# Performance work log

Hardware: AMD Instinct MI355X
Metric: run time of the kernel (lower is better)

## Reference

```python
import jax, jax.numpy as jnp
import numpy as np

NUM_HEADS = 8
FREQ_RATIO = 0.5

def setup_inputs() -> dict:
    key = jax.random.key(0)
    ks = jax.random.split(key, 4)
    B, T, J, C = 16, 256, 17, 512
    x = jax.random.normal(ks[0], (B, T, J, C), jnp.float32)
    w_qkv = jax.random.normal(ks[1], (3 * C, C), jnp.float32) * 0.02
    w_proj = jax.random.normal(ks[2], (C, C), jnp.float32) * 0.02
    b_proj = jnp.zeros((C,), jnp.float32)
    freq_gate = jnp.ones((1,), jnp.float32)
    return {"x": x, "w_qkv": w_qkv, "w_proj": w_proj, "b_proj": b_proj, "freq_gate": freq_gate}

def reference(x, w_qkv, w_proj, b_proj, freq_gate):
    B, T, J, C = x.shape
    H = NUM_HEADS
    hd = C // H
    scale = hd ** (-0.5)
    # qkv projection (no bias): [B,T,J,3,H,hd] -> [3,B,H,T,J,hd]
    qkv = (x @ w_qkv.T).reshape(B, T, J, 3, H, hd)
    qkv = jnp.transpose(qkv, (3, 0, 4, 1, 2, 5))
    q, k, v = qkv[0], qkv[1], qkv[2]
    # temporal layout: [B,H,J,T,hd]
    qt = jnp.swapaxes(q, 2, 3)
    kt = jnp.swapaxes(k, 2, 3)
    vt = jnp.swapaxes(v, 2, 3)
    # ---- time-domain temporal attention ----
    attn = jax.nn.softmax(jnp.einsum('bhjtd,bhjsd->bhjts', qt, kt) * scale, axis=-1)
    x_time = jnp.einsum('bhjts,bhjsd->bhjtd', attn, vt)
    x_time = jnp.transpose(x_time, (0, 3, 2, 1, 4)).reshape(B, T, J, C)
    # ---- frequency-domain temporal attention ----
    qf = jnp.fft.rfft(qt, axis=3)
    kf = jnp.fft.rfft(kt, axis=3)
    vf = jnp.fft.rfft(vt, axis=3)
    f_full = T // 2 + 1
    keep = max(1, int(f_full * FREQ_RATIO))  # low-frequency crop
    qf, kf, vf = qf[:, :, :, :keep], kf[:, :, :, :keep], vf[:, :, :, :keep]
    af = jnp.einsum('bhjfd,bhjgd->bhjfg', qf, jnp.conj(kf)) * scale  # complex [B,H,J,keep,keep]
    af = jax.nn.softmax(af.real, axis=-1) + 1j * jax.nn.softmax(af.imag, axis=-1)
    xf = jnp.einsum('bhjfg,bhjgd->bhjfd', af, vf)
    xf = jnp.pad(xf, ((0, 0), (0, 0), (0, 0), (0, f_full - keep), (0, 0)))  # zero-pad high freqs
    x_freq = jnp.fft.irfft(xf, n=T, axis=3)
    x_freq = jnp.transpose(x_freq, (0, 3, 2, 1, 4)).reshape(B, T, J, C)
    # ---- gated combine + output projection ----
    gate = jax.nn.sigmoid(freq_gate)[0]
    out = gate * x_freq + (1.0 - gate) * x_time
    return out @ w_proj.T + b_proj
```

## Files before the change

### kernel.cpp

```cpp
#include <hip/hip_runtime.h>
#include <hip/hip_fp16.h>
#include <math.h>

#define NB 16
#define TT 256
#define JJ 17
#define CC 512
#define HH 8
#define HD 64
#define MROWS (NB*TT*JJ)
#define QTILE 16384
#define NTILES (NB*HH*JJ)
#define NQKV 35651584

#define W0 0.0245436926061702596f

typedef __attribute__((ext_vector_type(8))) short i16x8;
typedef __attribute__((ext_vector_type(8))) _Float16 f16x8;
typedef __attribute__((ext_vector_type(4))) float f32x4;

__device__ __forceinline__ unsigned short f2h(float f) {
    return (unsigned short)__half_as_ushort(__float2half(f));
}
__device__ __forceinline__ float h2f(unsigned short u) {
    return __half2float(__ushort_as_half(u));
}

#define GLD16(gp, lp) __builtin_amdgcn_global_load_lds( \
    (__attribute__((address_space(1))) void*)(gp), \
    (__attribute__((address_space(3))) void*)(lp), 16, 0, 0)

__global__ __launch_bounds__(256) void conv16_k(
    const float* __restrict__ s, unsigned short* __restrict__ d, int n8)
{
    for (int i = blockIdx.x*256 + threadIdx.x; i < n8; i += gridDim.x*256) {
        float4 a = ((const float4*)s)[i*2];
        float4 b = ((const float4*)s)[i*2+1];
        i16x8 h;
        h[0] = (short)f2h(a.x); h[1] = (short)f2h(a.y);
        h[2] = (short)f2h(a.z); h[3] = (short)f2h(a.w);
        h[4] = (short)f2h(b.x); h[5] = (short)f2h(b.y);
        h[6] = (short)f2h(b.z); h[7] = (short)f2h(b.w);
        ((i16x8*)d)[i] = h;
    }
}

__global__ __launch_bounds__(256) void prep_k(
    const float* __restrict__ wq, const float* __restrict__ wp,
    unsigned short* __restrict__ wqh, unsigned short* __restrict__ wph,
    unsigned short* __restrict__ Whi, unsigned short* __restrict__ Wlo,
    unsigned short* __restrict__ WIhi)
{
    const int b = blockIdx.x;
    const int tid = threadIdx.x;
    if (b < 512) {
        const float* s = (b < 384) ? wq : wp;
        unsigned short* d = (b < 384) ? wqh : wph;
        int i = (b < 384 ? b : b - 384)*256 + tid;
        float4 a = ((const float4*)s)[i*2];
        float4 bb = ((const float4*)s)[i*2+1];
        i16x8 h;
        h[0] = (short)f2h(a.x); h[1] = (short)f2h(a.y);
        h[2] = (short)f2h(a.z); h[3] = (short)f2h(a.w);
        h[4] = (short)f2h(bb.x); h[5] = (short)f2h(bb.y);
        h[6] = (short)f2h(bb.z); h[7] = (short)f2h(bb.w);
        ((i16x8*)d)[i] = h;
    } else if (b < 640) {
        const int r = b - 512;
        const int t = tid;
        int idx = ((r & 63) * t) & 255;
        float sv, cv;
        sincosf(W0 * (float)idx, &sv, &cv);
        float val = (r < 64) ? cv : -sv;
        unsigned short h = f2h(val);
        Whi[r*256 + t] = h;
        Wlo[r*256 + t] = f2h(val - h2f(h));
    } else {
        int idx = (b - 640)*256 + tid;
        int t = idx >> 7;
        int f = idx & 127;
        int fr = f & 63;
        int ii = (t * fr) & 255;
        float sv, cv;
        sincosf(W0 * (float)ii, &sv, &cv);
        float cf = (fr == 0 && f < 64) ? 0.5f : 1.f;
        float val = ((f < 64) ? cv : -sv) * cf * (2.f / 256.f);
        WIhi[t*128 + f] = f2h(val);
    }
}

__global__ __launch_bounds__(256) void gemm_qkv_k(
    const unsigned short* __restrict__ A, const unsigned short* __restrict__ B,
    unsigned short* __restrict__ qp, unsigned short* __restrict__ kp,
    unsigned short* __restrict__ vp)
{
    __shared__ unsigned short Sh[128*128];
    unsigned short* Ah = Sh;
    unsigned short* Bh = Sh + 128*64;
    const int tid = threadIdx.x;
    const int lane = tid & 63;
    const int lo = lane & 15, hi = lane >> 4;
    const int wv = tid >> 6;
    const int wr = wv >> 1, wc = wv & 1;
    const int bid = blockIdx.x;
    const int wrk = (bid & 7) * 816 + (bid >> 3);
    const int col0 = (wrk % 12) * 128;
    const int row0 = (wrk / 12) * 128;

    f32x4 acc[4][4];
    #pragma unroll
    for (int rb = 0; rb < 4; ++rb)
        #pragma unroll
        for (int cb = 0; cb < 4; ++cb) acc[rb][cb] = (f32x4){0.f,0.f,0.f,0.f};

    for (int k0 = 0; k0 < 512; k0 += 64) {
        #pragma unroll
        for (int c = 0; c < 4; ++c) {
            int e = c*2048 + tid*8;
            int r = e >> 6, cc = e & 63;
            int ccs = cc ^ ((r & 7) << 3);
            size_t offA = (size_t)(row0 + r)*512 + k0 + ccs;
            size_t offB = (size_t)(col0 + r)*512 + k0 + ccs;
            GLD16(A + offA, (char*)Ah + c*4096 + tid*16);
            GLD16(B + offB, (char*)Bh + c*4096 + tid*16);
        }
        __syncthreads();
        #pragma unroll
        for (int ks = 0; ks < 2; ++ks) {
            f16x8 af[4], bf[4];
            #pragma unroll
            for (int rb = 0; rb < 4; ++rb) {
                int row = wr*64 + rb*16 + lo;
                int col = (ks*32 + hi*8) ^ ((row & 7) << 3);
                af[rb] = *(const f16x8*)&Ah[row*64 + col];
            }
            #pragma unroll
            for (int cb = 0; cb < 4; ++cb) {
                int row = wc*64 + cb*16 + lo;
                int col = (ks*32 + hi*8) ^ ((row & 7) << 3);
                bf[cb] = *(const f16x8*)&Bh[row*64 + col];
            }
            #pragma unroll
            for (int rb = 0; rb < 4; ++rb)
                #pragma unroll
                for (int cb = 0; cb < 4; ++cb)
                    acc[rb][cb] = __builtin_amdgcn_mfma_f32_16x16x32_f16(
                        af[rb], bf[cb], acc[rb][cb], 0, 0, 0);
        }
        __syncthreads();
    }

    #pragma unroll
    for (int cb = 0; cb < 4; ++cb) {
        int n0 = col0 + wc*64 + cb*16;
        float scl = ((n0 >> 9) == 0) ? 0.125f : 1.f;
        #pragma unroll
        for (int rb = 0; rb < 4; ++rb)
            #pragma unroll
            for (int r = 0; r < 4; ++r) {
                int row = wr*64 + rb*16 + hi*4 + r;
                int col = wc*64 + cb*16 + lo;
                Sh[row*128 + (col ^ ((row & 7) << 3))] = f2h(acc[rb][cb][r]*scl);
            }
    }
    __syncthreads();

    {
        const int grp = lane >> 3;
        const int d0 = (lane & 7) * 8;
        #pragma unroll
        for (int it = 0; it < 8; ++it) {
            int p = it*32 + wv*8 + grp;
            int row = p >> 1;
            int half = p & 1;
            int m = row0 + row;
            int bb = m / (TT*JJ);
            int rem = m - bb*(TT*JJ);
            int t = rem / JJ;
            int j = rem - t*JJ;
            int n0 = col0 + half*64;
            int g = n0 >> 9;
            unsigned short* dst0 = (g == 0) ? qp : (g == 1) ? kp : vp;
            int h = (n0 >> 6) & 7;
            unsigned short* dst = dst0 +
                ((((size_t)bb*HH + h)*JJ + j)*TT + t)*HD + d0;
            i16x8 vls = *(const i16x8*)&Sh[row*128 + ((half*64 + d0) ^ ((row & 7) << 3))];
            *(i16x8*)dst = vls;
        }
    }
}

__global__ __launch_bounds__(256) void gemm_proj_k(
    const unsigned short* __restrict__ A, const unsigned short* __restrict__ B,
    const float* __restrict__ bias, float* __restrict__ out)
{
    __shared__ unsigned short Ah[128*64];
    __shared__ unsigned short Bh[128*64];
    const int tid = threadIdx.x;
    const int lane = tid & 63;
    const int lo = lane & 15, hi = lane >> 4;
    const int wv = tid >> 6;
    const int wr = wv >> 1, wc = wv & 1;
    const int bid = blockIdx.x;
    const int wrk = (bid & 7) * 272 + (bid >> 3);
    const int col0 = (wrk % 4) * 128;
    const int row0 = (wrk / 4) * 128;

    f32x4 acc[4][4];
    #pragma unroll
    for (int rb = 0; rb < 4; ++rb)
        #pragma unroll
        for (int cb = 0; cb < 4; ++cb) acc[rb][cb] = (f32x4){0.f,0.f,0.f,0.f};

    for (int k0 = 0; k0 < 512; k0 += 64) {
        #pragma unroll
        for (int c = 0; c < 4; ++c) {
            int e = c*2048 + tid*8;
            int r = e >> 6, cc = e & 63;
            int ccs = cc ^ ((r & 7) << 3);
            size_t offA = (size_t)(row0 + r)*512 + k0 + ccs;
            size_t offB = (size_t)(col0 + r)*512 + k0 + ccs;
            GLD16(A + offA, (char*)Ah + c*4096 + tid*16);
            GLD16(B + offB, (char*)Bh + c*4096 + tid*16);
        }
        __syncthreads();
        #pragma unroll
        for (int ks = 0; ks < 2; ++ks) {
            f16x8 af[4], bf[4];
            #pragma unroll
            for (int rb = 0; rb < 4; ++rb) {
                int row = wr*64 + rb*16 + lo;
                int col = (ks*32 + hi*8) ^ ((row & 7) << 3);
                af[rb] = *(const f16x8*)&Ah[row*64 + col];
            }
            #pragma unroll
            for (int cb = 0; cb < 4; ++cb) {
                int row = wc*64 + cb*16 + lo;
                int col = (ks*32 + hi*8) ^ ((row & 7) << 3);
                bf[cb] = *(const f16x8*)&Bh[row*64 + col];
            }
            #pragma unroll
            for (int rb = 0; rb < 4; ++rb)
                #pragma unroll
                for (int cb = 0; cb < 4; ++cb)
                    acc[rb][cb] = __builtin_amdgcn_mfma_f32_16x16x32_f16(
                        af[rb], bf[cb], acc[rb][cb], 0, 0, 0);
        }
        __syncthreads();
    }

    #pragma unroll
    for (int cb = 0; cb < 4; ++cb) {
        int n = col0 + wc*64 + cb*16 + lo;
        float bv = bias[n];
        #pragma unroll
        for (int rb = 0; rb < 4; ++rb)
            #pragma unroll
            for (int r = 0; r < 4; ++r) {
                int m = row0 + wr*64 + rb*16 + hi*4 + r;
                out[(size_t)m*512 + n] = acc[rb][cb][r] + bv;
            }
    }
}

#define PPW 40

__global__ __launch_bounds__(256, 3) void attn_time_k(
    const unsigned short* __restrict__ q, const unsigned short* __restrict__ k,
    const unsigned short* __restrict__ v, const float* __restrict__ fg,
    unsigned short* __restrict__ y)
{
    __shared__ unsigned short VT[64 * 256];
    __shared__ unsigned short PL[4 * 64 * PPW];

    const int bid = blockIdx.x;
    const int b = bid / (HH*JJ);
    const int h = (bid / JJ) % HH;
    const int j = bid % JJ;
    const size_t base = (size_t)bid * QTILE;

    const int tid = threadIdx.x;
    const int w = tid >> 6;
    const int lane = tid & 63;
    const int lo = lane & 15;
    const int hi = lane >> 4;

    {
        const unsigned short* vptr = v + base + (size_t)tid * HD;
        #pragma unroll
        for (int d0 = 0; d0 < 64; d0 += 8) {
            i16x8 vv = *(const i16x8*)(vptr + d0);
            #pragma unroll
            for (int e = 0; e < 8; ++e) {
                int row = d0 + e;
                VT[row*256 + (tid ^ ((row & 7) << 3))] = (unsigned short)vv[e];
            }
        }
    }
    __syncthreads();

    f16x8 qf[4][2];
    #pragma unroll
    for (int rb = 0; rb < 4; ++rb)
        #pragma unroll
        for (int dc = 0; dc < 2; ++dc)
            qf[rb][dc] = *(const f16x8*)(q + base + (size_t)(w*64 + rb*16 + lo)*HD + dc*32 + hi*8);

    f32x4 o[4][4];
    #pragma unroll
    for (int rb = 0; rb < 4; ++rb)
        #pragma unroll
        for (int cd = 0; cd < 4; ++cd) o[rb][cd] = (f32x4){0.f,0.f,0.f,0.f};
    float rs[4][4];
    #pragma unroll
    for (int rb = 0; rb < 4; ++rb)
        #pragma unroll
        for (int r = 0; r < 4; ++r) rs[rb][r] = 0.f;

    unsigned short* Pw = PL + w * 64 * PPW;

    for (int st = 0; st < 8; ++st) {
        const int s0 = st * 32;
        f16x8 kf[2][2];
        #pragma unroll
        for (int cb = 0; cb < 2; ++cb)
            #pragma unroll
            for (int dc = 0; dc < 2; ++dc)
                kf[cb][dc] = *(const f16x8*)(k + base + (size_t)(s0 + cb*16 + lo)*HD + dc*32 + hi*8);

        #pragma unroll
        for (int rb = 0; rb < 4; ++rb) {
            #pragma unroll
            for (int cb = 0; cb < 2; ++cb) {
                f32x4 acc = (f32x4){0.f,0.f,0.f,0.f};
                acc = __builtin_amdgcn_mfma_f32_16x16x32_f16(qf[rb][0], kf[cb][0], acc, 0, 0, 0);
                acc = __builtin_amdgcn_mfma_f32_16x16x32_f16(qf[rb][1], kf[cb][1], acc, 0, 0, 0);
                #pragma unroll
                for (int r = 0; r < 4; ++r) {
                    float p = __expf(acc[r]);
                    rs[rb][r] += p;
                    Pw[(rb*16 + hi*4 + r)*PPW + cb*16 + lo] = f2h(p);
                }
            }
        }

        f16x8 pa[4];
        #pragma unroll
        for (int rb = 0; rb < 4; ++rb)
            pa[rb] = *(const f16x8*)&Pw[(rb*16 + lo)*PPW + hi*8];
        f16x8 bv[4];
        #pragma unroll
        for (int cd = 0; cd < 4; ++cd) {
            int row = cd*16 + lo;
            bv[cd] = *(const f16x8*)&VT[row*256 + ((s0 + hi*8) ^ ((row & 7) << 3))];
        }
        #pragma unroll
        for (int rb = 0; rb < 4; ++rb)
            #pragma unroll
            for (int cd = 0; cd < 4; ++cd)
                o[rb][cd] = __builtin_amdgcn_mfma_f32_16x16x32_f16(pa[rb], bv[cd], o[rb][cd], 0, 0, 0);
    }

    #pragma unroll
    for (int off = 1; off < 16; off <<= 1)
        #pragma unroll
        for (int rb = 0; rb < 4; ++rb)
            #pragma unroll
            for (int r = 0; r < 4; ++r)
                rs[rb][r] += __shfl_xor(rs[rb][r], off, 64);

    const float gate = 1.f / (1.f + __expf(-fg[0]));
    const float wt = 1.f - gate;
    #pragma unroll
    for (int rb = 0; rb < 4; ++rb) {
        #pragma unroll
        for (int r = 0; r < 4; ++r) {
            const int t = w*64 + rb*16 + hi*4 + r;
            const float sc = wt / rs[rb][r];
            unsigned short* yp = y + (((size_t)b*TT + t)*JJ + j)*CC + h*HD;
            #pragma unroll
            for (int cd = 0; cd < 4; ++cd)
                yp[cd*16 + lo] = f2h(o[rb][cd][r] * sc);
        }
    }
}

#define XP 280

__global__ __launch_bounds__(256) void dft_k(
    unsigned short* __restrict__ planes, const unsigned short* __restrict__ Whi,
    const unsigned short* __restrict__ Wlo)
{
    __shared__ unsigned short Xh[64*XP];
    unsigned short* src = planes + (size_t)blockIdx.y*NQKV + (size_t)blockIdx.x*QTILE;
    const int tid = threadIdx.x;
    const int w = tid >> 6;
    const int lane = tid & 63;
    const int qd = (tid >> 4) & 3;
    const int rr = tid & 15;
    const int lo = lane & 15, hi = lane >> 4;

    #pragma unroll
    for (int p = 0; p < 16; ++p) {
        const int t = p*16 + 4*w + qd;
        ushort4 x4 = *(const ushort4*)&src[t*64 + 4*rr];
        unsigned int a0 = x4.x, a1 = x4.y, a2 = x4.z, a3 = x4.w;
        unsigned int t01 = (unsigned)__shfl_xor((int)((qd&1) ? a0 : a1), 16, 64);
        unsigned int t23 = (unsigned)__shfl_xor((int)((qd&1) ? a2 : a3), 16, 64);
        if (qd&1) { a0 = t01; a2 = t23; } else { a1 = t01; a3 = t23; }
        unsigned int u01 = (unsigned)__shfl_xor((int)((qd&2) ? a0 : a2), 32, 64);
        unsigned int u23 = (unsigned)__shfl_xor((int)((qd&2) ? a1 : a3), 32, 64);
        if (qd&2) { a0 = u01; a1 = u23; } else { a2 = u01; a3 = u23; }
        const int dd = 4*rr + qd;
        const int tb = p*16 + 4*w;
        ushort4 hv;
        hv.x = (unsigned short)a0; hv.y = (unsigned short)a1;
        hv.z = (unsigned short)a2; hv.w = (unsigned short)a3;
        *(ushort4*)&Xh[dd*XP + tb] = hv;
    }
    __syncthreads();

    f32x4 acc[2][4];
    #pragma unroll
    for (int rb = 0; rb < 2; ++rb)
        #pragma unroll
        for (int cd = 0; cd < 4; ++cd) acc[rb][cd] = (f32x4){0.f,0.f,0.f,0.f};

    for (int ks = 0; ks < 8; ++ks) {
        const int k0 = ks*32;
        f16x8 ah[2], al[2];
        #pragma unroll
        for (int rb = 0; rb < 2; ++rb) {
            int r = w*32 + rb*16 + lo;
            ah[rb] = *(const f16x8*)&Whi[r*256 + k0 + hi*8];
            al[rb] = *(const f16x8*)&Wlo[r*256 + k0 + hi*8];
        }
        f16x8 bh[4];
        #pragma unroll
        for (int cd = 0; cd < 4; ++cd) {
            int d = cd*16 + lo;
            bh[cd] = *(const f16x8*)&Xh[d*XP + k0 + hi*8];
        }
        #pragma unroll
        for (int rb = 0; rb < 2; ++rb)
            #pragma unroll
            for (int cd = 0; cd < 4; ++cd) {
                acc[rb][cd] = __builtin_amdgcn_mfma_f32_16x16x32_f16(
                    ah[rb], bh[cd], acc[rb][cd], 0, 0, 0);
                acc[rb][cd] = __builtin_amdgcn_mfma_f32_16x16x32_f16(
                    al[rb], bh[cd], acc[rb][cd], 0, 0, 0);
            }
    }

    #pragma unroll
    for (int rb = 0; rb < 2; ++rb) {
        #pragma unroll
        for (int r = 0; r < 4; ++r) {
            int row = w*32 + rb*16 + hi*4 + r;
            unsigned short* dst = (row < 64) ? (src + row*64)
                                             : (src + 4096 + (row-64)*64);
            #pragma unroll
            for (int cd = 0; cd < 4; ++cd)
                dst[cd*16 + lo] = f2h(acc[rb][cd][r]);
        }
    }
}

#define FQP 72
#define XFP 136

__global__ __launch_bounds__(256) void freqtail_k(
    const unsigned short* __restrict__ qfp, const unsigned short* __restrict__ kfp,
    const unsigned short* __restrict__ vfp, const unsigned short* __restrict__ WIhi,
    const float* __restrict__ fg, unsigned short* __restrict__ y)
{
    __shared__ unsigned short S1[128*FQP];
    __shared__ unsigned short S2[128*FQP];

    const int tid = threadIdx.x;
    const int tile = blockIdx.x;
    const int b = tile / (HH*JJ);
    const int h = (tile / JJ) % HH;
    const int j = tile % JJ;
    const unsigned short* qf = qfp + (size_t)tile * QTILE;
    const unsigned short* kf = kfp + (size_t)tile * QTILE;
    const unsigned short* vf = vfp + (size_t)tile * QTILE;

    const int w = tid >> 6;
    const int lane = tid & 63;
    const int lo = lane & 15, hi = lane >> 4;
    const int comp = w >> 1;
    const int fr0 = (w & 1) * 32;

    #pragma unroll
    for (int p = 0; p < 4; ++p) {
        int e8 = (p*256 + tid) * 8;
        int row = e8 >> 6, col = e8 & 63;
        *(i16x8*)&S1[row*FQP + col] = *(const i16x8*)(qf + e8);
        *(i16x8*)&S2[row*FQP + col] = *(const i16x8*)(kf + e8);
    }
    __syncthreads();

    f32x4 accA[2][4], accB[2][4];
    #pragma unroll
    for (int rb = 0; rb < 2; ++rb)
        #pragma unroll
        for (int cb = 0; cb < 4; ++cb) {
            accA[rb][cb] = (f32x4){0.f,0.f,0.f,0.f};
            accB[rb][cb] = (f32x4){0.f,0.f,0.f,0.f};
        }
    #pragma unroll
    for (int ks = 0; ks < 2; ++ks) {
        f16x8 qA[2], qB[2];
        #pragma unroll
        for (int rb = 0; rb < 2; ++rb) {
            int fr = fr0 + rb*16 + lo;
            qA[rb] = *(const f16x8*)&S1[(comp*64 + fr)*FQP + ks*32 + hi*8];
            qB[rb] = *(const f16x8*)&S1[((1-comp)*64 + fr)*FQP + ks*32 + hi*8];
        }
        f16x8 kr[4], ki[4];
        #pragma unroll
        for (int cb = 0; cb < 4; ++cb) {
            int g = cb*16 + lo;
            kr[cb] = *(const f16x8*)&S2[g*FQP + ks*32 + hi*8];
            ki[cb] = *(const f16x8*)&S2[(64 + g)*FQP + ks*32 + hi*8];
        }
        #pragma unroll
        for (int rb = 0; rb < 2; ++rb)
            #pragma unroll
            for (int cb = 0; cb < 4; ++cb) {
                accA[rb][cb] = __builtin_amdgcn_mfma_f32_16x16x32_f16(
                    qA[rb], kr[cb], accA[rb][cb], 0, 0, 0);
                accB[rb][cb] = __builtin_amdgcn_mfma_f32_16x16x32_f16(
                    qB[rb], ki[cb], accB[rb][cb], 0, 0, 0);
            }
    }
    __syncthreads();

    const float sgn = comp ? -1.f : 1.f;
    float pv[2][4][4];
    float inv[2][4];
    #pragma unroll
    for (int rb = 0; rb < 2; ++rb) {
        #pragma unroll
        for (int r = 0; r < 4; ++r) {
            float m = -3.0e38f;
            #pragma unroll
            for (int cb = 0; cb < 4; ++cb) {
                float vv = accA[rb][cb][r] + sgn*accB[rb][cb][r];
                pv[rb][cb][r] = vv;
                m = fmaxf(m, vv);
            }
            #pragma unroll
            for (int off = 1; off < 16; off <<= 1)
                m = fmaxf(m, __shfl_xor(m, off, 64));
            float s = 0.f;
            #pragma unroll
            for (int cb = 0; cb < 4; ++cb) {
                float e = __expf(pv[rb][cb][r] - m);
                pv[rb][cb][r] = e;
                s += e;
            }
            #pragma unroll
            for (int off = 1; off < 16; off <<= 1)
                s += __shfl_xor(s, off, 64);
            inv[rb][r] = 1.f / s;
        }
    }
    #pragma unroll
    for (int rb = 0; rb < 2; ++rb)
        #pragma unroll
        for (int r = 0; r < 4; ++r)
            #pragma unroll
            for (int cb = 0; cb < 4; ++cb)
                S1[(w*32 + rb*16 + hi*4 + r)*FQP + cb*16 + lo] =
                    f2h(pv[rb][cb][r] * inv[rb][r]);

    #pragma unroll
    for (int p = 0; p < 4; ++p) {
        int e8 = (p*256 + tid) * 8;
        int srow = e8 >> 6;
        int c2 = srow >> 6, g = srow & 63, d0 = e8 & 63;
        i16x8 vv = *(const i16x8*)(vf + e8);
        #pragma unroll
        for (int e = 0; e < 8; ++e)
            S2[(c2*64 + d0 + e)*FQP + g] = (unsigned short)vv[e];
    }
    __syncthreads();

    f32x4 xA[2][4], xB[2][4];
    #pragma unroll
    for (int rb = 0; rb < 2; ++rb)
        #pragma unroll
        for (int cd = 0; cd < 4; ++cd) {
            xA[rb][cd] = (f32x4){0.f,0.f,0.f,0.f};
            xB[rb][cd] = (f32x4){0.f,0.f,0.f,0.f};
        }
    #pragma unroll
    for (int ks = 0; ks < 2; ++ks) {
        f16x8 pA[2], pB[2];
        #pragma unroll
        for (int rb = 0; rb < 2; ++rb) {
            int fr = fr0 + rb*16 + lo;
            pA[rb] = *(const f16x8*)&S1[fr*FQP + ks*32 + hi*8];
            pB[rb] = *(const f16x8*)&S1[(64 + fr)*FQP + ks*32 + hi*8];
        }
        f16x8 bA[4], bB[4];
        #pragma unroll
        for (int cd = 0; cd < 4; ++cd) {
            int d = cd*16 + lo;
            bA[cd] = *(const f16x8*)&S2[(comp*64 + d)*FQP + ks*32 + hi*8];
            bB[cd] = *(const f16x8*)&S2[((1-comp)*64 + d)*FQP + ks*32 + hi*8];
        }
        #pragma unroll
        for (int rb = 0; rb < 2; ++rb)
            #pragma unroll
            for (int cd = 0; cd < 4; ++cd) {
                xA[rb][cd] = __builtin_amdgcn_mfma_f32_16x16x32_f16(
                    pA[rb], bA[cd], xA[rb][cd], 0, 0, 0);
                xB[rb][cd] = __builtin_amdgcn_mfma_f32_16x16x32_f16(
                    pB[rb], bB[cd], xB[rb][cd], 0, 0, 0);
            }
    }
    __syncthreads();

    const float sgn2 = comp ? 1.f : -1.f;
    unsigned short* XT = S1;
    #pragma unroll
    for (int rb = 0; rb < 2; ++rb)
        #pragma unroll
        for (int cd = 0; cd < 4; ++cd)
            #pragma unroll
            for (int r = 0; r < 4; ++r) {
                int f = fr0 + rb*16 + hi*4 + r;
                int d = cd*16 + lo;
                XT[d*XFP + comp*64 + f] =
                    f2h(xA[rb][cd][r] + sgn2*xB[rb][cd][r]);
            }
    __syncthreads();

    f32x4 acc[4][4];
    #pragma unroll
    for (int rb = 0; rb < 4; ++rb)
        #pragma unroll
        for (int cd = 0; cd < 4; ++cd) acc[rb][cd] = (f32x4){0.f,0.f,0.f,0.f};

    #pragma unroll
    for (int ks = 0; ks < 4; ++ks) {
        const int k0 = ks*32;
        f16x8 ah[4];
        #pragma unroll
        for (int rb = 0; rb < 4; ++rb) {
            int row = w*64 + rb*16 + lo;
            ah[rb] = *(const f16x8*)&WIhi[row*128 + k0 + hi*8];
        }
        f16x8 bt[4];
        #pragma unroll
        for (int cd = 0; cd < 4; ++cd) {
            int d = cd*16 + lo;
            bt[cd] = *(const f16x8*)&XT[d*XFP + k0 + hi*8];
        }
        #pragma unroll
        for (int rb = 0; rb < 4; ++rb)
            #pragma unroll
            for (int cd = 0; cd < 4; ++cd)
                acc[rb][cd] = __builtin_amdgcn_mfma_f32_16x16x32_f16(
                    ah[rb], bt[cd], acc[rb][cd], 0, 0, 0);
    }

    const float gate = 1.f / (1.f + __expf(-fg[0]));
    #pragma unroll
    for (int rb = 0; rb < 4; ++rb) {
        #pragma unroll
        for (int r = 0; r < 4; ++r) {
            int t = w*64 + rb*16 + hi*4 + r;
            unsigned short* yp = y + (((size_t)b*TT + t)*JJ + j)*CC + h*HD;
            #pragma unroll
            for (int cd = 0; cd < 4; ++cd) {
                int d = cd*16 + lo;
                yp[d] = f2h(fmaf(gate, acc[rb][cd][r], h2f(yp[d])));
            }
        }
    }
}

extern "C" void kernel_launch(void* const* d_in, const int* in_sizes, int n_in,
                              void* d_out, int out_size, void* d_ws, size_t ws_size,
                              hipStream_t stream) {
    const float* x      = (const float*)d_in[0];
    const float* w_qkv  = (const float*)d_in[1];
    const float* w_proj = (const float*)d_in[2];
    const float* b_proj = (const float*)d_in[3];
    const float* fg     = (const float*)d_in[4];
    float* out = (float*)d_out;

    unsigned short* qp = (unsigned short*)d_ws;
    unsigned short* kp = qp + NQKV;
    unsigned short* vp = kp + NQKV;
    unsigned short* xh = vp + NQKV;
    unsigned short* y  = xh + NQKV;
    unsigned short* wph = y + NQKV;
    unsigned short* wqh = (unsigned short*)d_out;
    unsigned short* Whi  = wqh + 1536*512;
    unsigned short* Wlo  = Whi + 128*256;
    unsigned short* WIhi = Wlo + 128*256;

    conv16_k<<<2048, 256, 0, stream>>>(x, xh, NQKV/8);
    prep_k<<<768, 256, 0, stream>>>(w_qkv, w_proj, wqh, wph, Whi, Wlo, WIhi);

    gemm_qkv_k<<<6528, 256, 0, stream>>>(xh, wqh, qp, kp, vp);
    attn_time_k<<<NTILES, 256, 0, stream>>>(qp, kp, vp, fg, y);
    dft_k<<<dim3(NTILES, 3), 256, 0, stream>>>(qp, Whi, Wlo);
    freqtail_k<<<NTILES, 256, 0, stream>>>(qp, kp, vp, WIhi, fg, y);

    gemm_proj_k<<<2176, 256, 0, stream>>>(y, wph, b_proj, out);
}
```

Measured before the change: 586.1 us.

## Fuse forward DFT into frequency-attention kernel with swizzled shared memory

Removes the separate dft_k launch. The truncated DFT of each q/k/v tile is now computed inside freqtail_k, streaming T in two halves through a swizzled LDS buffer, so the in-place global write and reread of the frequency planes disappear. The padded LDS layouts are replaced by XOR swizzles to cut bank conflicts, and the V transform skips the low-precision correction MFMA. The cost is more LDS per block, possibly lower occupancy, and slightly lower precision for V.

Result: no change. 588.5 us (+0.4%).

```diff
diff --git a/kernel.cpp b/kernel.cpp
--- a/kernel.cpp
+++ b/kernel.cpp
@@ -29,6 +29,9 @@
 #define GLD16(gp, lp) __builtin_amdgcn_global_load_lds( \
     (__attribute__((address_space(1))) void*)(gp), \
     (__attribute__((address_space(3))) void*)(lp), 16, 0, 0)
+
+#define SWZ(row, col) ((row)*64 + ((col) ^ (((row) & 7) << 3)))
+#define TSW(row, col) ((row)*128 + ((col) ^ (((row) & 7) << 3)))
 
 __global__ __launch_bounds__(256) void conv16_k(
     const float* __restrict__ s, unsigned short* __restrict__ d, int n8)
@@ -385,106 +388,92 @@
     }
 }
 
-#define XP 280
-
-__global__ __launch_bounds__(256) void dft_k(
-    unsigned short* __restrict__ planes, const unsigned short* __restrict__ Whi,
-    const unsigned short* __restrict__ Wlo)
+__device__ __forceinline__ void dft_plane(
+    const unsigned short* __restrict__ src, const unsigned short* __restrict__ Whi,
+    const unsigned short* __restrict__ Wlo, unsigned short* XTMP,
+    int tid, f32x4 dacc[2][4], bool useLo)
 {
-    __shared__ unsigned short Xh[64*XP];
-    unsigned short* src = planes + (size_t)blockIdx.y*NQKV + (size_t)blockIdx.x*QTILE;
-    const int tid = threadIdx.x;
     const int w = tid >> 6;
     const int lane = tid & 63;
+    const int lo = lane & 15, hi = lane >> 4;
     const int qd = (tid >> 4) & 3;
     const int rr = tid & 15;
-    const int lo = lane & 15, hi = lane >> 4;
-
-    #pragma unroll
-    for (int p = 0; p < 16; ++p) {
-        const int t = p*16 + 4*w + qd;
-        ushort4 x4 = *(const ushort4*)&src[t*64 + 4*rr];
-        unsigned int a0 = x4.x, a1 = x4.y, a2 = x4.z, a3 = x4.w;
-        unsigned int t01 = (unsigned)__shfl_xor((int)((qd&1) ? a0 : a1), 16, 64);
-        unsigned int t23 = (unsigned)__shfl_xor((int)((qd&1) ? a2 : a3), 16, 64);
-        if (qd&1) { a0 = t01; a2 = t23; } else { a1 = t01; a3 = t23; }
-        unsigned int u01 = (unsigned)__shfl_xor((int)((qd&2) ? a0 : a2), 32, 64);
-        unsigned int u23 = (unsigned)__shfl_xor((int)((qd&2) ? a1 : a3), 32, 64);
-        if (qd&2) { a0 = u01; a1 = u23; } else { a2 = u01; a3 = u23; }
-        const int dd = 4*rr + qd;
-        const int tb = p*16 + 4*w;
-        ushort4 hv;
-        hv.x = (unsigned short)a0; hv.y = (unsigned short)a1;
-        hv.z = (unsigned short)a2; hv.w = (unsigned short)a3;
-        *(ushort4*)&Xh[dd*XP + tb] = hv;
-    }
-    __syncthreads();
-
-    f32x4 acc[2][4];
+
     #pragma unroll
     for (int rb = 0; rb < 2; ++rb)
         #pragma unroll
-        for (int cd = 0; cd < 4; ++cd) acc[rb][cd] = (f32x4){0.f,0.f,0.f,0.f};
-
-    for (int ks = 0; ks < 8; ++ks) {
-        const int k0 = ks*32;
-        f16x8 ah[2], al[2];
-        #pragma unroll
-        for (int rb = 0; rb < 2; ++rb) {
-            int r = w*32 + rb*16 + lo;
-            ah[rb] = *(const f16x8*)&Whi[r*256 + k0 + hi*8];
-            al[rb] = *(const f16x8*)&Wlo[r*256 + k0 + hi*8];
-        }
-        f16x8 bh[4];
-        #pragma unroll
-        for (int cd = 0; cd < 4; ++cd) {
-            int d = cd*16 + lo;
-            bh[cd] = *(const f16x8*)&Xh[d*XP + k0 + hi*8];
-        }
-        #pragma unroll
-        for (int rb = 0; rb < 2; ++rb)
+        for (int cd = 0; cd < 4; ++cd) dacc[rb][cd] = (f32x4){0.f,0.f,0.f,0.f};
+
+    for (int hf = 0; hf < 2; ++hf) {
+        __syncthreads();
+        #pragma unroll
+        for (int p = 0; p < 8; ++p) {
+            const int tloc = p*16 + 4*w + qd;
+            const int t = hf*128 + tloc;
+            ushort4 x4 = *(const ushort4*)&src[t*64 + 4*rr];
+            unsigned int a0 = x4.x, a1 = x4.y, a2 = x4.z, a3 = x4.w;
+            unsigned int t01 = (unsigned)__shfl_xor((int)((qd&1) ? a0 : a1), 16, 64);
+            unsigned int t23 = (unsigned)__shfl_xor((int)((qd&1) ? a2 : a3), 16, 64);
+            if (qd&1) { a0 = t01; a2 = t23; } else { a1 = t01; a3 = t23; }
+            unsigned int u01 = (unsigned)__shfl_xor((int)((qd&2) ? a0 : a2), 32, 64);
+            unsigned int u23 = (unsigned)__shfl_xor((int)((qd&2) ? a1 : a3), 32, 64);
+            if (qd&2) { a0 = u01; a1 = u23; } else { a2 = u01; a3 = u23; }
+            const int dd = 4*rr + qd;
+            const int tb = p*16 + 4*w;
+            ushort4 hv;
+            hv.x = (unsigned short)a0; hv.y = (unsigned short)a1;
+            hv.z = (unsigned short)a2; hv.w = (unsigned short)a3;
+            *(ushort4*)&XTMP[dd*128 + (tb ^ ((dd & 7) << 3))] = hv;
+        }
+        __syncthreads();
+        #pragma unroll
+        for (int ks = 0; ks < 4; ++ks) {
+            const int k0 = ks*32;
+            f16x8 ah[2], al[2];
+            #pragma unroll
+            for (int rb = 0; rb < 2; ++rb) {
+                int rw = w*32 + rb*16 + lo;
+                ah[rb] = *(const f16x8*)&Whi[rw*256 + hf*128 + k0 + hi*8];
+                if (useLo) al[rb] = *(const f16x8*)&Wlo[rw*256 + hf*128 + k0 + hi*8];
+            }
+            f16x8 bh[4];
             #pragma unroll
             for (int cd = 0; cd < 4; ++cd) {
-                acc[rb][cd] = __builtin_amdgcn_mfma_f32_16x16x32_f16(
-                    ah[rb], bh[cd], acc[rb][cd], 0, 0, 0);
-                acc[rb][cd] = __builtin_amdgcn_mfma_f32_16x16x32_f16(
-                    al[rb], bh[cd], acc[rb][cd], 0, 0, 0);
-            }
-    }
-
-    #pragma unroll
-    for (int rb = 0; rb < 2; ++rb) {
-        #pragma unroll
-        for (int r = 0; r < 4; ++r) {
-            int row = w*32 + rb*16 + hi*4 + r;
-            unsigned short* dst = (row < 64) ? (src + row*64)
-                                             : (src + 4096 + (row-64)*64);
-            #pragma unroll
-            for (int cd = 0; cd < 4; ++cd)
-                dst[cd*16 + lo] = f2h(acc[rb][cd][r]);
-        }
-    }
-}
-
-#define FQP 72
-#define XFP 136
+                int d = cd*16 + lo;
+                bh[cd] = *(const f16x8*)&XTMP[TSW(d, k0 + hi*8)];
+            }
+            #pragma unroll
+            for (int rb = 0; rb < 2; ++rb)
+                #pragma unroll
+                for (int cd = 0; cd < 4; ++cd) {
+                    dacc[rb][cd] = __builtin_amdgcn_mfma_f32_16x16x32_f16(
+                        ah[rb], bh[cd], dacc[rb][cd], 0, 0, 0);
+                    if (useLo)
+                        dacc[rb][cd] = __builtin_amdgcn_mfma_f32_16x16x32_f16(
+                            al[rb], bh[cd], dacc[rb][cd], 0, 0, 0);
+                }
+        }
+    }
+}
 
 __global__ __launch_bounds__(256) void freqtail_k(
-    const unsigned short* __restrict__ qfp, const unsigned short* __restrict__ kfp,
-    const unsigned short* __restrict__ vfp, const unsigned short* __restrict__ WIhi,
+    const unsigned short* __restrict__ qp, const unsigned short* __restrict__ kp,
+    const unsigned short* __restrict__ vp, const unsigned short* __restrict__ Whi,
+    const unsigned short* __restrict__ Wlo, const unsigned short* __restrict__ WIhi,
     const float* __restrict__ fg, unsigned short* __restrict__ y)
 {
-    __shared__ unsigned short S1[128*FQP];
-    __shared__ unsigned short S2[128*FQP];
+    __shared__ unsigned short S1[128*64];
+    __shared__ unsigned short S2[128*64];
+    __shared__ unsigned short XTMP[64*128];
 
     const int tid = threadIdx.x;
     const int tile = blockIdx.x;
     const int b = tile / (HH*JJ);
     const int h = (tile / JJ) % HH;
     const int j = tile % JJ;
-    const unsigned short* qf = qfp + (size_t)tile * QTILE;
-    const unsigned short* kf = kfp + (size_t)tile * QTILE;
-    const unsigned short* vf = vfp + (size_t)tile * QTILE;
+    const unsigned short* qsrc = qp + (size_t)tile * QTILE;
+    const unsigned short* ksrc = kp + (size_t)tile * QTILE;
+    const unsigned short* vsrc = vp + (size_t)tile * QTILE;
 
     const int w = tid >> 6;
     const int lane = tid & 63;
@@ -492,13 +481,29 @@
     const int comp = w >> 1;
     const int fr0 = (w & 1) * 32;
 
-    #pragma unroll
-    for (int p = 0; p < 4; ++p) {
-        int e8 = (p*256 + tid) * 8;
-        int row = e8 >> 6, col = e8 & 63;
-        *(i16x8*)&S1[row*FQP + col] = *(const i16x8*)(qf + e8);
-        *(i16x8*)&S2[row*FQP + col] = *(const i16x8*)(kf + e8);
-    }
+    f32x4 dacc[2][4];
+
+    dft_plane(qsrc, Whi, Wlo, XTMP, tid, dacc, true);
+    #pragma unroll
+    for (int rb = 0; rb < 2; ++rb)
+        #pragma unroll
+        for (int cd = 0; cd < 4; ++cd)
+            #pragma unroll
+            for (int r = 0; r < 4; ++r) {
+                int row = w*32 + rb*16 + hi*4 + r;
+                S1[SWZ(row, cd*16 + lo)] = f2h(dacc[rb][cd][r]);
+            }
+
+    dft_plane(ksrc, Whi, Wlo, XTMP, tid, dacc, true);
+    #pragma unroll
+    for (int rb = 0; rb < 2; ++rb)
+        #pragma unroll
+        for (int cd = 0; cd < 4; ++cd)
+            #pragma unroll
+            for (int r = 0; r < 4; ++r) {
+                int row = w*32 + rb*16 + hi*4 + r;
+                S2[SWZ(row, cd*16 + lo)] = f2h(dacc[rb][cd][r]);
+            }
     __syncthreads();
 
     f32x4 accA[2][4], accB[2][4];
@@ -515,15 +520,15 @@
         #pragma unroll
         for (int rb = 0; rb < 2; ++rb) {
             int fr = fr0 + rb*16 + lo;
-            qA[rb] = *(const f16x8*)&S1[(comp*64 + fr)*FQP + ks*32 + hi*8];
-            qB[rb] = *(const f16x8*)&S1[((1-comp)*64 + fr)*FQP + ks*32 + hi*8];
+            qA[rb] = *(const f16x8*)&S1[SWZ(comp*64 + fr, ks*32 + hi*8)];
+            qB[rb] = *(const f16x8*)&S1[SWZ((1-comp)*64 + fr, ks*32 + hi*8)];
         }
         f16x8 kr[4], ki[4];
         #pragma unroll
         for (int cb = 0; cb < 4; ++cb) {
             int g = cb*16 + lo;
-            kr[cb] = *(const f16x8*)&S2[g*FQP + ks*32 + hi*8];
-            ki[cb] = *(const f16x8*)&S2[(64 + g)*FQP + ks*32 + hi*8];
+            kr[cb] = *(const f16x8*)&S2[SWZ(g, ks*32 + hi*8)];
+            ki[cb] = *(const f16x8*)&S2[SWZ(64 + g, ks*32 + hi*8)];
         }
         #pragma unroll
         for (int rb = 0; rb < 2; ++rb)
@@ -573,19 +578,20 @@
         for (int r = 0; r < 4; ++r)
             #pragma unroll
             for (int cb = 0; cb < 4; ++cb)
-                S1[(w*32 + rb*16 + hi*4 + r)*FQP + cb*16 + lo] =
+                S1[SWZ(w*32 + rb*16 + hi*4 + r, cb*16 + lo)] =
                     f2h(pv[rb][cb][r] * inv[rb][r]);
 
-    #pragma unroll
-    for (int p = 0; p < 4; ++p) {
-        int e8 = (p*256 + tid) * 8;
-        int srow = e8 >> 6;
-        int c2 = srow >> 6, g = srow & 63, d0 = e8 & 63;
-        i16x8 vv = *(const i16x8*)(vf + e8);
-        #pragma unroll
-        for (int e = 0; e < 8; ++e)
-            S2[(c2*64 + d0 + e)*FQP + g] = (unsigned short)vv[e];
-    }
+    dft_plane(vsrc, Whi, Wlo, XTMP, tid, dacc, false);
+    #pragma unroll
+    for (int rb = 0; rb < 2; ++rb)
+        #pragma unroll
+        for (int cd = 0; cd < 4; ++cd)
+            #pragma unroll
+            for (int r = 0; r < 4; ++r) {
+                int gr = w*32 + rb*16 + hi*4 + r;
+                int rowv = (gr >> 6)*64 + cd*16 + lo;
+                S2[SWZ(rowv, gr & 63)] = f2h(dacc[rb][cd][r]);
+            }
     __syncthreads();
 
     f32x4 xA[2][4], xB[2][4];
@@ -602,15 +608,15 @@
         #pragma unroll
         for (int rb = 0; rb < 2; ++rb) {
             int fr = fr0 + rb*16 + lo;
-            pA[rb] = *(const f16x8*)&S1[fr*FQP + ks*32 + hi*8];
-            pB[rb] = *(const f16x8*)&S1[(64 + fr)*FQP + ks*32 + hi*8];
+            pA[rb] = *(const f16x8*)&S1[SWZ(fr, ks*32 + hi*8)];
+            pB[rb] = *(const f16x8*)&S1[SWZ(64 + fr, ks*32 + hi*8)];
         }
         f16x8 bA[4], bB[4];
         #pragma unroll
         for (int cd = 0; cd < 4; ++cd) {
             int d = cd*16 + lo;
-            bA[cd] = *(const f16x8*)&S2[(comp*64 + d)*FQP + ks*32 + hi*8];
-            bB[cd] = *(const f16x8*)&S2[((1-comp)*64 + d)*FQP + ks*32 + hi*8];
+            bA[cd] = *(const f16x8*)&S2[SWZ(comp*64 + d, ks*32 + hi*8)];
+            bB[cd] = *(const f16x8*)&S2[SWZ((1-comp)*64 + d, ks*32 + hi*8)];
         }
         #pragma unroll
         for (int rb = 0; rb < 2; ++rb)
@@ -634,7 +640,7 @@
             for (int r = 0; r < 4; ++r) {
                 int f = fr0 + rb*16 + hi*4 + r;
                 int d = cd*16 + lo;
-                XT[d*XFP + comp*64 + f] =
+                XT[TSW(d, comp*64 + f)] =
                     f2h(xA[rb][cd][r] + sgn2*xB[rb][cd][r]);
             }
     __syncthreads();
@@ -658,7 +664,7 @@
         #pragma unroll
         for (int cd = 0; cd < 4; ++cd) {
             int d = cd*16 + lo;
-            bt[cd] = *(const f16x8*)&XT[d*XFP + k0 + hi*8];
+            bt[cd] = *(const f16x8*)&XT[TSW(d, k0 + hi*8)];
         }
         #pragma unroll
         for (int rb = 0; rb < 4; ++rb)
@@ -710,8 +716,7 @@
 
     gemm_qkv_k<<<6528, 256, 0, stream>>>(xh, wqh, qp, kp, vp);
     attn_time_k<<<NTILES, 256, 0, stream>>>(qp, kp, vp, fg, y);
-    dft_k<<<dim3(NTILES, 3), 256, 0, stream>>>(qp, Whi, Wlo);
-    freqtail_k<<<NTILES, 256, 0, stream>>>(qp, kp, vp, WIhi, fg, y);
+    freqtail_k<<<NTILES, 256, 0, stream>>>(qp, kp, vp, Whi, Wlo, WIhi, fg, y);
 
     gemm_proj_k<<<2176, 256, 0, stream>>>(y, wph, b_proj, out);
 }
```

## Widen QKV GEMM tile to 128x256 and drop low-part DFT MFMAs for V

Applied to the files above, without the earlier changes.

The QKV projection GEMM now computes a 128x256 output tile per block, so each A tile loaded into LDS is reused across two 128-column B tiles and the grid is halved. The epilogue writes the two halves in turn through the same LDS buffer, and the row index decoding is hoisted out of that loop. Separately, the DFT kernel skips the low-order twiddle correction (Wlo) MFMAs for the V plane, halving its matrix work there at some cost in precision. The larger tile doubles accumulator registers (launch bounds now request 3 blocks per CU), which may reduce occupancy or cause spills.

Measured after the change: 672.8 us. 1.15x slower.

```diff
diff --git a/kernel.cpp b/kernel.cpp
--- a/kernel.cpp
+++ b/kernel.cpp
@@ -89,29 +89,33 @@
     }
 }
 
-__global__ __launch_bounds__(256) void gemm_qkv_k(
+__global__ __launch_bounds__(256, 3) void gemm_qkv_k(
     const unsigned short* __restrict__ A, const unsigned short* __restrict__ B,
     unsigned short* __restrict__ qp, unsigned short* __restrict__ kp,
     unsigned short* __restrict__ vp)
 {
-    __shared__ unsigned short Sh[128*128];
-    unsigned short* Ah = Sh;
-    unsigned short* Bh = Sh + 128*64;
+    __shared__ unsigned short LDS[3*128*64];
+    unsigned short* Ah = LDS;
+    unsigned short* B1 = LDS + 128*64;
+    unsigned short* B2 = LDS + 2*128*64;
     const int tid = threadIdx.x;
     const int lane = tid & 63;
     const int lo = lane & 15, hi = lane >> 4;
     const int wv = tid >> 6;
     const int wr = wv >> 1, wc = wv & 1;
     const int bid = blockIdx.x;
-    const int wrk = (bid & 7) * 816 + (bid >> 3);
-    const int col0 = (wrk % 12) * 128;
-    const int row0 = (wrk / 12) * 128;
-
-    f32x4 acc[4][4];
-    #pragma unroll
-    for (int rb = 0; rb < 4; ++rb)
-        #pragma unroll
-        for (int cb = 0; cb < 4; ++cb) acc[rb][cb] = (f32x4){0.f,0.f,0.f,0.f};
+    const int wrk = (bid & 7) * 408 + (bid >> 3);
+    const int cp   = wrk % 6;
+    const int row0 = (wrk / 6) * 128;
+    const int col0 = cp * 256;
+
+    f32x4 acc[2][4][4];
+    #pragma unroll
+    for (int p = 0; p < 2; ++p)
+        #pragma unroll
+        for (int rb = 0; rb < 4; ++rb)
+            #pragma unroll
+            for (int cb = 0; cb < 4; ++cb) acc[p][rb][cb] = (f32x4){0.f,0.f,0.f,0.f};
 
     for (int k0 = 0; k0 < 512; k0 += 64) {
         #pragma unroll
@@ -119,15 +123,14 @@
             int e = c*2048 + tid*8;
             int r = e >> 6, cc = e & 63;
             int ccs = cc ^ ((r & 7) << 3);
-            size_t offA = (size_t)(row0 + r)*512 + k0 + ccs;
-            size_t offB = (size_t)(col0 + r)*512 + k0 + ccs;
-            GLD16(A + offA, (char*)Ah + c*4096 + tid*16);
-            GLD16(B + offB, (char*)Bh + c*4096 + tid*16);
+            GLD16(A + (size_t)(row0 + r)*512 + k0 + ccs, (char*)Ah + c*4096 + tid*16);
+            GLD16(B + (size_t)(col0 + r)*512 + k0 + ccs, (char*)B1 + c*4096 + tid*16);
+            GLD16(B + (size_t)(col0 + 128 + r)*512 + k0 + ccs, (char*)B2 + c*4096 + tid*16);
         }
         __syncthreads();
         #pragma unroll
         for (int ks = 0; ks < 2; ++ks) {
-            f16x8 af[4], bf[4];
+            f16x8 af[4];
             #pragma unroll
             for (int rb = 0; rb < 4; ++rb) {
                 int row = wr*64 + rb*16 + lo;
@@ -135,58 +138,78 @@
                 af[rb] = *(const f16x8*)&Ah[row*64 + col];
             }
             #pragma unroll
-            for (int cb = 0; cb < 4; ++cb) {
-                int row = wc*64 + cb*16 + lo;
-                int col = (ks*32 + hi*8) ^ ((row & 7) << 3);
-                bf[cb] = *(const f16x8*)&Bh[row*64 + col];
-            }
-            #pragma unroll
-            for (int rb = 0; rb < 4; ++rb)
+            for (int p = 0; p < 2; ++p) {
+                const unsigned short* Bp = p ? B2 : B1;
+                f16x8 bf[4];
                 #pragma unroll
-                for (int cb = 0; cb < 4; ++cb)
-                    acc[rb][cb] = __builtin_amdgcn_mfma_f32_16x16x32_f16(
-                        af[rb], bf[cb], acc[rb][cb], 0, 0, 0);
+                for (int cb = 0; cb < 4; ++cb) {
+                    int row = wc*64 + cb*16 + lo;
+                    int col = (ks*32 + hi*8) ^ ((row & 7) << 3);
+                    bf[cb] = *(const f16x8*)&Bp[row*64 + col];
+                }
+                #pragma unroll
+                for (int rb = 0; rb < 4; ++rb)
+                    #pragma unroll
+                    for (int cb = 0; cb < 4; ++cb)
+                        acc[p][rb][cb] = __builtin_amdgcn_mfma_f32_16x16x32_f16(
+                            af[rb], bf[cb], acc[p][rb][cb], 0, 0, 0);
+            }
         }
         __syncthreads();
     }
 
-    #pragma unroll
-    for (int cb = 0; cb < 4; ++cb) {
-        int n0 = col0 + wc*64 + cb*16;
-        float scl = ((n0 >> 9) == 0) ? 0.125f : 1.f;
-        #pragma unroll
-        for (int rb = 0; rb < 4; ++rb)
-            #pragma unroll
-            for (int r = 0; r < 4; ++r) {
-                int row = wr*64 + rb*16 + hi*4 + r;
-                int col = wc*64 + cb*16 + lo;
-                Sh[row*128 + (col ^ ((row & 7) << 3))] = f2h(acc[rb][cb][r]*scl);
-            }
-    }
-    __syncthreads();
-
+    int bbA[8], ttA[8], jjA[8];
     {
         const int grp = lane >> 3;
-        const int d0 = (lane & 7) * 8;
         #pragma unroll
         for (int it = 0; it < 8; ++it) {
-            int p = it*32 + wv*8 + grp;
-            int row = p >> 1;
-            int half = p & 1;
+            int p2 = it*32 + wv*8 + grp;
+            int row = p2 >> 1;
             int m = row0 + row;
             int bb = m / (TT*JJ);
             int rem = m - bb*(TT*JJ);
             int t = rem / JJ;
-            int j = rem - t*JJ;
-            int n0 = col0 + half*64;
-            int g = n0 >> 9;
-            unsigned short* dst0 = (g == 0) ? qp : (g == 1) ? kp : vp;
-            int h = (n0 >> 6) & 7;
-            unsigned short* dst = dst0 +
-                ((((size_t)bb*HH + h)*JJ + j)*TT + t)*HD + d0;
-            i16x8 vls = *(const i16x8*)&Sh[row*128 + ((half*64 + d0) ^ ((row & 7) << 3))];
-            *(i16x8*)dst = vls;
-        }
+            bbA[it] = bb; ttA[it] = t; jjA[it] = rem - t*JJ;
+        }
+    }
+
+    unsigned short* Sh = LDS;
+    #pragma unroll
+    for (int p = 0; p < 2; ++p) {
+        const int col0p = col0 + p*128;
+        #pragma unroll
+        for (int cb = 0; cb < 4; ++cb) {
+            int n0 = col0p + wc*64 + cb*16;
+            float scl = ((n0 >> 9) == 0) ? 0.125f : 1.f;
+            #pragma unroll
+            for (int rb = 0; rb < 4; ++rb)
+                #pragma unroll
+                for (int r = 0; r < 4; ++r) {
+                    int row = wr*64 + rb*16 + hi*4 + r;
+                    int col = wc*64 + cb*16 + lo;
+                    Sh[row*128 + (col ^ ((row & 7) << 3))] = f2h(acc[p][rb][cb][r]*scl);
+                }
+        }
+        __syncthreads();
+        {
+            const int grp = lane >> 3;
+            const int d0 = (lane & 7) * 8;
+            #pragma unroll
+            for (int it = 0; it < 8; ++it) {
+                int p2 = it*32 + wv*8 + grp;
+                int row = p2 >> 1;
+                int half = p2 & 1;
+                int n0 = col0p + half*64;
+                int g = n0 >> 9;
+                unsigned short* dst0 = (g == 0) ? qp : (g == 1) ? kp : vp;
+                int h = (n0 >> 6) & 7;
+                unsigned short* dst = dst0 +
+                    ((((size_t)bbA[it]*HH + h)*JJ + jjA[it])*TT + ttA[it])*HD + d0;
+                i16x8 vls = *(const i16x8*)&Sh[row*128 + ((half*64 + d0) ^ ((row & 7) << 3))];
+                *(i16x8*)dst = vls;
+            }
+        }
+        __syncthreads();
     }
 }
 
@@ -393,6 +416,7 @@
 {
     __shared__ unsigned short Xh[64*XP];
     unsigned short* src = planes + (size_t)blockIdx.y*NQKV + (size_t)blockIdx.x*QTILE;
+    const bool useLo = (blockIdx.y != 2);
     const int tid = threadIdx.x;
     const int w = tid >> 6;
     const int lane = tid & 63;
@@ -433,7 +457,7 @@
         for (int rb = 0; rb < 2; ++rb) {
             int r = w*32 + rb*16 + lo;
             ah[rb] = *(const f16x8*)&Whi[r*256 + k0 + hi*8];
-            al[rb] = *(const f16x8*)&Wlo[r*256 + k0 + hi*8];
+            if (useLo) al[rb] = *(const f16x8*)&Wlo[r*256 + k0 + hi*8];
         }
         f16x8 bh[4];
         #pragma unroll
@@ -447,8 +471,9 @@
             for (int cd = 0; cd < 4; ++cd) {
                 acc[rb][cd] = __builtin_amdgcn_mfma_f32_16x16x32_f16(
                     ah[rb], bh[cd], acc[rb][cd], 0, 0, 0);
-                acc[rb][cd] = __builtin_amdgcn_mfma_f32_16x16x32_f16(
-                    al[rb], bh[cd], acc[rb][cd], 0, 0, 0);
+                if (useLo)
+                    acc[rb][cd] = __builtin_amdgcn_mfma_f32_16x16x32_f16(
+                        al[rb], bh[cd], acc[rb][cd], 0, 0, 0);
             }
     }
 
@@ -708,7 +733,7 @@
     conv16_k<<<2048, 256, 0, stream>>>(x, xh, NQKV/8);
     prep_k<<<768, 256, 0, stream>>>(w_qkv, w_proj, wqh, wph, Whi, Wlo, WIhi);
 
-    gemm_qkv_k<<<6528, 256, 0, stream>>>(xh, wqh, qp, kp, vp);
+    gemm_qkv_k<<<3264, 256, 0, stream>>>(xh, wqh, qp, kp, vp);
     attn_time_k<<<NTILES, 256, 0, stream>>>(qp, kp, vp, fg, y);
     dft_k<<<dim3(NTILES, 3), 256, 0, stream>>>(qp, Whi, Wlo);
     freqtail_k<<<NTILES, 256, 0, stream>>>(qp, kp, vp, WIhi, fg, y);
```
